# Kernel tuning notes

Hardware: AMD Instinct MI355X
Metric: run time of the kernel (lower is better)

## Reference

```python
import jax, jax.numpy as jnp
import numpy as np

H = 16   # num_heads
G = 4    # groups (code structurally requires 4)
DIM = 1024
HD = DIM // H // G  # 16


def setup_inputs() -> dict:
    key = jax.random.key(0)
    k1, k2, k3 = jax.random.split(key, 3)
    x = jax.random.normal(k1, (8, 4096, DIM), dtype=jnp.float32)
    w_qkvw = jax.random.normal(k2, (DIM, 4 * DIM), dtype=jnp.float32) * 0.02
    w_out = jax.random.normal(k3, (DIM, DIM), dtype=jnp.float32) * 0.02
    return {"x": x, "w_qkvw": w_qkvw, "w_out": w_out}


def reference(x, w_qkvw, w_out):
    B, S, dim = x.shape
    qkvw = x @ w_qkvw  # [B, S, 4*dim]
    # chunk into G groups along last dim -> G tensors of [B, S, dim] (G==4)
    chunks = jnp.split(qkvw, G, axis=-1)
    # each chunk split again into G sub-chunks of [B, S, dim/G]
    subs = [jnp.split(t, G, axis=-1) for t in chunks]
    # torch: q,k,v,w = [cat([qi,ki,vi,wi], dim=0) for qi,ki,vi,wi in zip(*subs)]
    q = jnp.concatenate([subs[i][0] for i in range(4)], axis=0)  # [4B, S, dim/G]
    k = jnp.concatenate([subs[i][1] for i in range(4)], axis=0)
    v = jnp.concatenate([subs[i][2] for i in range(4)], axis=0)
    w = jnp.concatenate([subs[i][3] for i in range(4)], axis=0)
    # faithful row-major reshape: [4B, S, dim/G] -> [4B, H, S, hd] -> transpose(1,2)
    def shp(t):
        return t.reshape(B * G, H, -1, HD).swapaxes(1, 2)  # [4B, S, H, hd]
    q, k, v = shp(q), shp(k), shp(v)
    w = w.reshape(B * G, H, -1, HD)  # [4B, H, S, hd]
    scale = HD ** -0.5
    scores = (q @ k.swapaxes(-2, -1)) * scale          # [4B, S, H, H]
    attn = jax.nn.softmax(scores, axis=-1)
    o = (attn @ v).swapaxes(1, 2).reshape(B, S, dim)   # [B, S, dim]
    return (o * w.reshape(B, S, dim)) @ w_out
```

## Files before the change

kernel.cpp:

```cpp
#include <hip/hip_runtime.h>
#include <hip/hip_bf16.h>
#include <stdint.h>


typedef __bf16 bf16;
typedef __bf16 bf16x8 __attribute__((ext_vector_type(8)));
typedef float f32x4 __attribute__((ext_vector_type(4)));

__device__ __forceinline__ void gload16(const bf16* g, bf16* l) {
  __builtin_amdgcn_global_load_lds(
      (const __attribute__((address_space(1))) void*)g,
      (__attribute__((address_space(3))) void*)l, 16, 0, 0);
}

#define BAR() asm volatile("s_barrier" ::: "memory")
#define SB() __builtin_amdgcn_sched_barrier(0)
#define LGKM0 asm volatile("s_waitcnt lgkmcnt(0)" ::: "memory")
#define PRIO1 __builtin_amdgcn_s_setprio(1)
#define PRIO0 __builtin_amdgcn_s_setprio(0)

#define READ_AX(dst, mq, AO)                                                  \
  {                                                                           \
    _Pragma("unroll") for (int i = 0; i < 4; ++i)                             \
        _Pragma("unroll") for (int kk = 0; kk < 2; ++kk)                      \
            dst[i][kk] = *(const bf16x8*)(lds + (AO) +                        \
                                          ((mq)*64 + i * 16 + fr) * 128 +     \
                                          ((kk * 64 + fkb) ^ xo));            \
  }
#define READ_B(nh, BO)                                                        \
  {                                                                           \
    _Pragma("unroll") for (int j = 0; j < 2; ++j)                             \
        _Pragma("unroll") for (int kk = 0; kk < 2; ++kk)                      \
            b[(nh)*2 + j][kk] = *(const bf16x8*)(lds + (BO) +                 \
                                                 (bro + (nh)*32 + j * 16 + fr) * 128 + \
                                                 ((kk * 64 + fkb) ^ xo));     \
  }
#define MFMA_Q(arr, mq, nh)                                                   \
  {                                                                           \
    _Pragma("unroll") for (int i = 0; i < 4; ++i)                             \
        _Pragma("unroll") for (int j = 0; j < 2; ++j) {                       \
      acc[(mq)*4 + i][(nh)*2 + j] = __builtin_amdgcn_mfma_f32_16x16x32_bf16(  \
          arr[i][0], b[(nh)*2 + j][0], acc[(mq)*4 + i][(nh)*2 + j], 0, 0, 0); \
      acc[(mq)*4 + i][(nh)*2 + j] = __builtin_amdgcn_mfma_f32_16x16x32_bf16(  \
          arr[i][1], b[(nh)*2 + j][1], acc[(mq)*4 + i][(nh)*2 + j], 0, 0, 0); \
    }                                                                         \
  }
#define STAGE_AH(h, X, base)                                                  \
  {                                                                           \
    const bf16* g = gA + ((h)*128) * 1024 + (X)*64;                           \
    gload16(g, (bf16*)(lds + (base) + (h)*16384 + wv * 1024));                \
    gload16(g + 64 * 1024, (bf16*)(lds + (base) + (h)*16384 + 8192 + wv * 1024)); \
  }
#define STAGE_BH(h, X)                                                        \
  {                                                                           \
    const int ro = 98304 + ((X)&1) * 32768 + (h)*16384;                       \
    const bf16* g = gB + ((h)*128) * 1024 + (X)*64;                           \
    gload16(g, (bf16*)(lds + ro + wv * 1024));                                \
    gload16(g + 64 * 1024, (bf16*)(lds + ro + 8192 + wv * 1024));             \
  }

template <typename OutT>
__global__ __launch_bounds__(512, 2)
void gemm256(const bf16* __restrict__ A, const bf16* __restrict__ BT,
             OutT* __restrict__ C, int N, int super) {
  constexpr int K = 1024;
  __shared__ __align__(16) char smem[163840];
  char* lds = smem;

  const int tid = threadIdx.x;
  const int lane = tid & 63;
  const int wv = tid >> 6;
  const int wr = wv >> 2;
  const int wc = wv & 3;

  const int gx = gridDim.x;
  const int nwg = gx * gridDim.y;
  const int bid = blockIdx.y * gx + blockIdx.x;
  const int xcd = bid & 7;
  const int l = bid >> 3;
  long trow, tcol;
  if (super) {
    const int s = l >> 5, i = l & 31;
    const int colS = gx >> 2;
    trow = xcd * 16 + (s / colS) * 8 + (i >> 2);
    tcol = (s % colS) * 4 + (i & 3);
  } else {
    const int swz = xcd * (nwg >> 3) + l;
    trow = swz / gx;
    tcol = swz % gx;
  }
  const long row0 = trow * 256;
  const long col0 = tcol * 256;

  const int srow = tid >> 3;
  const int scol = (((tid & 7) * 16) ^ ((srow & 7) << 4)) >> 1;
  const bf16* gA = A + (row0 + srow) * K + scol;
  const bf16* gB = BT + (col0 + srow) * K + scol;

  const int fr = lane & 15;
  const int fkb = (lane >> 4) * 16;
  const int xo = (fr & 7) << 4;
  const int bro = (wc & 1) * 64;

  bf16x8 a0[4][2], a1[4][2], b[4][2];
  f32x4 acc[8][4] = {};

  STAGE_AH(0, 0, 0); STAGE_AH(1, 0, 0);
  STAGE_BH(0, 0); STAGE_BH(1, 0);
  STAGE_AH(0, 1, 32768); STAGE_AH(1, 1, 32768);
  STAGE_BH(0, 1); STAGE_BH(1, 1);
  asm volatile("s_waitcnt vmcnt(8)" ::: "memory");
  SB(); BAR(); SB();
  READ_AX(a0, 0, wr * 16384);
  READ_B(0, 98304 + (wc >> 1) * 16384);
  SB();

  int ac0 = 0, ac1 = 32768, ac2 = 65536;
  for (int T = 0; T < 16; ++T) {
    const int aoff = ac0 + wr * 16384;
    const int aoffN = ac1 + wr * 16384;
    const int boff = 98304 + (T & 1) * 32768 + (wc >> 1) * 16384;
    const int boffN = 98304 + ((T + 1) & 1) * 32768 + (wc >> 1) * 16384;
    if (T < 14) STAGE_AH(0, T + 2, ac2);
    SB(); BAR(); LGKM0; SB();
    READ_B(1, boff); SB();
    PRIO1; MFMA_Q(a0, 0, 0); PRIO0; SB();
    if (T < 14) STAGE_AH(1, T + 2, ac2);
    SB(); BAR(); LGKM0; SB();
    PRIO1; MFMA_Q(a0, 0, 1); PRIO0; SB();
    READ_AX(a1, 1, aoff); SB();
    BAR();
    if (T < 14) {
      asm volatile("s_waitcnt vmcnt(4)" ::: "memory");
    } else if (T == 14) {
      asm volatile("s_waitcnt vmcnt(0)" ::: "memory");
    }
    LGKM0; SB();
    if (T < 14) STAGE_BH(0, T + 2);
    SB();
    PRIO1; MFMA_Q(a1, 1, 1); PRIO0; SB();
    if (T < 15) READ_AX(a0, 0, aoffN);
    SB();
    if (T < 14) STAGE_BH(1, T + 2);
    SB(); BAR(); SB();
    PRIO1; MFMA_Q(a1, 1, 0); PRIO0; SB();
    if (T < 15) READ_B(0, boffN);
    SB();
    const int t = ac0; ac0 = ac1; ac1 = ac2; ac2 = t;
  }

  const int crow = (lane >> 4) * 4;
  const int ccol = lane & 15;
  const long rb = row0 + wr * 128;
  const long cb = col0 + wc * 64;
#pragma unroll
  for (int m = 0; m < 8; ++m)
#pragma unroll
    for (int n = 0; n < 4; ++n)
#pragma unroll
      for (int i = 0; i < 4; ++i)
        C[(rb + m * 16 + crow + i) * (long)N + cb + n * 16 + ccol] =
            (OutT)acc[m][n][i];
}

__device__ __forceinline__ void load16f(const bf16* p, float* f) {
  const uint4* u = (const uint4*)p;
  uint4 a = u[0], b = u[1];
  uint32_t w[8] = {a.x, a.y, a.z, a.w, b.x, b.y, b.z, b.w};
#pragma unroll
  for (int j = 0; j < 8; ++j) {
    f[2 * j] = __uint_as_float(w[j] << 16);
    f[2 * j + 1] = __uint_as_float(w[j] & 0xffff0000u);
  }
}

__global__ __launch_bounds__(256)
void attn_fuse(const bf16* __restrict__ qkvw, bf16* __restrict__ ow,
               int b0, long bstride) {
  __shared__ bf16 data[16 * 1024];
  const int s_hi = blockIdx.x;
  const int g = blockIdx.y;
  const int bz = blockIdx.z;
  const int b = b0 + bz;
  const bf16* base = qkvw + (long)bz * bstride;
  const int tid = threadIdx.x;

#pragma unroll
  for (int i = 0; i < 8; ++i) {
    int c = tid + i * 256;
    int h = c >> 7;
    int col = (c & 127) * 8;
    *(uint4*)&data[h * 1024 + col] =
        *(const uint4*)(base + (long)(h * 256 + s_hi) * 4096 + g * 1024 + col);
  }
  __syncthreads();

  const int s_lo = tid >> 4;
  const int h1 = tid & 15;
  const int off = s_lo * 16;

  float q[16], p[16], o[16];
  load16f(&data[h1 * 1024 + off], q);

  float mx = -1e30f;
#pragma unroll
  for (int h2 = 0; h2 < 16; ++h2) {
    float kf[16];
    load16f(&data[h2 * 1024 + 256 + off], kf);
    float s = 0.f;
#pragma unroll
    for (int d = 0; d < 16; ++d) s += q[d] * kf[d];
    s *= 0.25f;
    p[h2] = s;
    mx = fmaxf(mx, s);
  }
  float sum = 0.f;
#pragma unroll
  for (int h2 = 0; h2 < 16; ++h2) {
    float e = __expf(p[h2] - mx);
    p[h2] = e;
    sum += e;
  }
  const float inv = 1.f / sum;
#pragma unroll
  for (int d = 0; d < 16; ++d) o[d] = 0.f;
#pragma unroll
  for (int h2 = 0; h2 < 16; ++h2) {
    float vf[16];
    load16f(&data[h2 * 1024 + 512 + off], vf);
    const float av = p[h2] * inv;
#pragma unroll
    for (int d = 0; d < 16; ++d) o[d] += av * vf[d];
  }
  float wf[16];
  load16f(&data[h1 * 1024 + 768 + off], wf);

  const int bp = g * 8 + b;
  const long R = (long)(bp >> 2) * 4096 + (bp & 3) * 1024 + h1 * 64 + (s_hi >> 2);
  const int cbo = (s_hi & 3) * 256 + off;
  union { uint4 u[2]; bf16 hh[16]; } st;
#pragma unroll
  for (int d = 0; d < 16; ++d) st.hh[d] = (bf16)(o[d] * wf[d]);
  uint4* dst = (uint4*)&ow[R * 1024 + cbo];
  dst[0] = st.u[0];
  dst[1] = st.u[1];
}

__global__ __launch_bounds__(256)
void cast_x_kernel(const float* __restrict__ in, bf16* __restrict__ out, long n4) {
  long i = (long)blockIdx.x * 256 + threadIdx.x;
  if (i >= n4) return;
  float4 v = ((const float4*)in)[i];
  union { uint2 d; bf16 h[4]; } r;
  r.h[0] = (bf16)v.x; r.h[1] = (bf16)v.y; r.h[2] = (bf16)v.z; r.h[3] = (bf16)v.w;
  ((uint2*)out)[i] = r.d;
}

__global__ __launch_bounds__(256)
void tcast_kernel(const float* __restrict__ in, bf16* __restrict__ out, int R, int C) {
  __shared__ float t[64][65];
  const int c0 = blockIdx.x * 64, r0 = blockIdx.y * 64;
  const int lr = threadIdx.x >> 6;
  const int lc = threadIdx.x & 63;
#pragma unroll
  for (int i = 0; i < 16; ++i)
    t[lr + i * 4][lc] = in[(long)(r0 + lr + i * 4) * C + c0 + lc];
  __syncthreads();
#pragma unroll
  for (int i = 0; i < 16; ++i) {
    int oc = lr + i * 4;
    out[(long)(c0 + oc) * R + r0 + lc] = (bf16)t[lc][oc];
  }
}

extern "C" void kernel_launch(void* const* d_in, const int* in_sizes, int n_in,
                              void* d_out, int out_size, void* d_ws, size_t ws_size,
                              hipStream_t stream) {
  const float* x = (const float*)d_in[0];
  const float* w_qkvw = (const float*)d_in[1];
  const float* w_out = (const float*)d_in[2];
  float* out = (float*)d_out;

  char* ws = (char*)d_ws;
  size_t off = 0;
  bf16* x_bf = (bf16*)(ws + off); off += (size_t)32768 * 1024 * 2;
  bf16* bt1  = (bf16*)(ws + off); off += (size_t)4096 * 1024 * 2;
  bf16* bt2  = (bf16*)(ws + off); off += (size_t)1024 * 1024 * 2;
  bf16* owb  = (bf16*)(ws + off); off += (size_t)32768 * 1024 * 2;
  bf16* qk   = (bf16*)(ws + off);
  const size_t rem = ws_size > off ? ws_size - off : 0;
  const size_t full_need = (size_t)32768 * 4096 * 2;

  cast_x_kernel<<<32768, 256, 0, stream>>>(x, x_bf, (long)8388608);
  tcast_kernel<<<dim3(64, 16), 256, 0, stream>>>(w_qkvw, bt1, 1024, 4096);
  tcast_kernel<<<dim3(16, 16), 256, 0, stream>>>(w_out, bt2, 1024, 1024);

  if (rem >= full_need) {
    gemm256<bf16><<<dim3(16, 128), 512, 0, stream>>>(x_bf, bt1, qk, 4096, 1);
    attn_fuse<<<dim3(256, 4, 8), 256, 0, stream>>>(qk, owb, 0, (long)4096 * 4096);
  } else {
    for (int b = 0; b < 8; ++b) {
      gemm256<bf16><<<dim3(16, 16), 512, 0, stream>>>(
          x_bf + (size_t)b * 4096 * 1024, bt1, qk, 4096, 0);
      attn_fuse<<<dim3(256, 4, 1), 256, 0, stream>>>(qk, owb, b, 0);
    }
  }
  gemm256<float><<<dim3(4, 128), 512, 0, stream>>>(owb, bt2, out, 1024, 1);
}
```

Measured before the change: 464.7 us.

## Restructure GEMM main loop into 8-phase ping-pong schedule with smaller LDS

Replaces the 3-stage A / 2-stage B LDS ring (160 KB) with a 2-stage double buffer for both A and B (128 KB). The K loop is unrolled by two tiles and split into eight MFMA quadrants, each followed by a barrier, with global-to-LDS staging interleaved at finer granularity. The aim is to cut LDS footprint, which may let two workgroups fit per CU, and to overlap loads with MFMA more evenly. The cost is a shallower prefetch depth and more barriers per K step, which can expose memory latency.

```diff
diff --git a/kernel.cpp b/kernel.cpp
--- a/kernel.cpp
+++ b/kernel.cpp
@@ -16,47 +16,41 @@
 #define BAR() asm volatile("s_barrier" ::: "memory")
 #define SB() __builtin_amdgcn_sched_barrier(0)
 #define LGKM0 asm volatile("s_waitcnt lgkmcnt(0)" ::: "memory")
+#define VM4 asm volatile("s_waitcnt vmcnt(4)" ::: "memory")
+#define VM0 asm volatile("s_waitcnt vmcnt(0)" ::: "memory")
 #define PRIO1 __builtin_amdgcn_s_setprio(1)
 #define PRIO0 __builtin_amdgcn_s_setprio(0)
 
-#define READ_AX(dst, mq, AO)                                                  \
+#define READ_A8(dst, base, mq)                                                \
   {                                                                           \
     _Pragma("unroll") for (int i = 0; i < 4; ++i)                             \
         _Pragma("unroll") for (int kk = 0; kk < 2; ++kk)                      \
-            dst[i][kk] = *(const bf16x8*)(lds + (AO) +                        \
+            dst[i][kk] = *(const bf16x8*)(lds + (base) + ahalf +              \
                                           ((mq)*64 + i * 16 + fr) * 128 +     \
                                           ((kk * 64 + fkb) ^ xo));            \
   }
-#define READ_B(nh, BO)                                                        \
+#define READ_B4(base, nh)                                                     \
   {                                                                           \
-    _Pragma("unroll") for (int j = 0; j < 2; ++j)                             \
+    _Pragma("unroll") for (int j2 = 0; j2 < 2; ++j2)                          \
         _Pragma("unroll") for (int kk = 0; kk < 2; ++kk)                      \
-            b[(nh)*2 + j][kk] = *(const bf16x8*)(lds + (BO) +                 \
-                                                 (bro + (nh)*32 + j * 16 + fr) * 128 + \
-                                                 ((kk * 64 + fkb) ^ xo));     \
+            b[(nh)*2 + j2][kk] = *(const bf16x8*)(lds + (base) + bhalf +      \
+                                                  (bro + (nh)*32 + j2 * 16 + fr) * 128 + \
+                                                  ((kk * 64 + fkb) ^ xo));    \
   }
 #define MFMA_Q(arr, mq, nh)                                                   \
   {                                                                           \
     _Pragma("unroll") for (int i = 0; i < 4; ++i)                             \
-        _Pragma("unroll") for (int j = 0; j < 2; ++j) {                       \
-      acc[(mq)*4 + i][(nh)*2 + j] = __builtin_amdgcn_mfma_f32_16x16x32_bf16(  \
-          arr[i][0], b[(nh)*2 + j][0], acc[(mq)*4 + i][(nh)*2 + j], 0, 0, 0); \
-      acc[(mq)*4 + i][(nh)*2 + j] = __builtin_amdgcn_mfma_f32_16x16x32_bf16(  \
-          arr[i][1], b[(nh)*2 + j][1], acc[(mq)*4 + i][(nh)*2 + j], 0, 0, 0); \
+        _Pragma("unroll") for (int j2 = 0; j2 < 2; ++j2) {                    \
+      acc[(mq)*4 + i][(nh)*2 + j2] = __builtin_amdgcn_mfma_f32_16x16x32_bf16( \
+          arr[i][0], b[(nh)*2 + j2][0], acc[(mq)*4 + i][(nh)*2 + j2], 0, 0, 0); \
+      acc[(mq)*4 + i][(nh)*2 + j2] = __builtin_amdgcn_mfma_f32_16x16x32_bf16( \
+          arr[i][1], b[(nh)*2 + j2][1], acc[(mq)*4 + i][(nh)*2 + j2], 0, 0, 0); \
     }                                                                         \
   }
-#define STAGE_AH(h, X, base)                                                  \
+#define STAGE(gsrc, lbase)                                                    \
   {                                                                           \
-    const bf16* g = gA + ((h)*128) * 1024 + (X)*64;                           \
-    gload16(g, (bf16*)(lds + (base) + (h)*16384 + wv * 1024));                \
-    gload16(g + 64 * 1024, (bf16*)(lds + (base) + (h)*16384 + 8192 + wv * 1024)); \
-  }
-#define STAGE_BH(h, X)                                                        \
-  {                                                                           \
-    const int ro = 98304 + ((X)&1) * 32768 + (h)*16384;                       \
-    const bf16* g = gB + ((h)*128) * 1024 + (X)*64;                           \
-    gload16(g, (bf16*)(lds + ro + wv * 1024));                                \
-    gload16(g + 64 * 1024, (bf16*)(lds + ro + 8192 + wv * 1024));             \
+    gload16((gsrc), (bf16*)(lds + (lbase) + wv * 1024));                      \
+    gload16((gsrc) + 64 * 1024, (bf16*)(lds + (lbase) + 8192 + wv * 1024));   \
   }
 
 template <typename OutT>
@@ -64,7 +58,7 @@
 void gemm256(const bf16* __restrict__ A, const bf16* __restrict__ BT,
              OutT* __restrict__ C, int N, int super) {
   constexpr int K = 1024;
-  __shared__ __align__(16) char smem[163840];
+  __shared__ __align__(16) char smem[131072];
   char* lds = smem;
 
   const int tid = threadIdx.x;
@@ -101,52 +95,62 @@
   const int fkb = (lane >> 4) * 16;
   const int xo = (fr & 7) << 4;
   const int bro = (wc & 1) * 64;
+  const int ahalf = wr * 16384;
+  const int bhalf = (wc >> 1) * 16384;
 
   bf16x8 a0[4][2], a1[4][2], b[4][2];
   f32x4 acc[8][4] = {};
 
-  STAGE_AH(0, 0, 0); STAGE_AH(1, 0, 0);
-  STAGE_BH(0, 0); STAGE_BH(1, 0);
-  STAGE_AH(0, 1, 32768); STAGE_AH(1, 1, 32768);
-  STAGE_BH(0, 1); STAGE_BH(1, 1);
-  asm volatile("s_waitcnt vmcnt(8)" ::: "memory");
+  STAGE(gA, 0); STAGE(gA + 131072, 16384);
+  STAGE(gB, 65536); STAGE(gB + 131072, 81920);
+  STAGE(gA + 64, 32768); STAGE(gA + 131072 + 64, 49152);
+  VM4;
   SB(); BAR(); SB();
-  READ_AX(a0, 0, wr * 16384);
-  READ_B(0, 98304 + (wc >> 1) * 16384);
-  SB();
-
-  int ac0 = 0, ac1 = 32768, ac2 = 65536;
-  for (int T = 0; T < 16; ++T) {
-    const int aoff = ac0 + wr * 16384;
-    const int aoffN = ac1 + wr * 16384;
-    const int boff = 98304 + (T & 1) * 32768 + (wc >> 1) * 16384;
-    const int boffN = 98304 + ((T + 1) & 1) * 32768 + (wc >> 1) * 16384;
-    if (T < 14) STAGE_AH(0, T + 2, ac2);
-    SB(); BAR(); LGKM0; SB();
-    READ_B(1, boff); SB();
-    PRIO1; MFMA_Q(a0, 0, 0); PRIO0; SB();
-    if (T < 14) STAGE_AH(1, T + 2, ac2);
-    SB(); BAR(); LGKM0; SB();
-    PRIO1; MFMA_Q(a0, 0, 1); PRIO0; SB();
-    READ_AX(a1, 1, aoff); SB();
-    BAR();
-    if (T < 14) {
-      asm volatile("s_waitcnt vmcnt(4)" ::: "memory");
-    } else if (T == 14) {
-      asm volatile("s_waitcnt vmcnt(0)" ::: "memory");
+
+  const bf16* gAm = gA;
+  const bf16* gBm = gB;
+  for (int j = 0; j < 8; ++j) {
+    const bool nl = (j < 7);
+    READ_A8(a0, 0, 0); READ_B4(65536, 0);
+    STAGE(gBm + 64, 98304);
+    SB(); BAR(); LGKM0; SB();
+    PRIO1; MFMA_Q(a0, 0, 0); PRIO0; SB(); BAR();
+    READ_A8(a1, 0, 1);
+    STAGE(gBm + 131072 + 64, 114688);
+    SB(); BAR(); LGKM0; SB();
+    PRIO1; MFMA_Q(a1, 1, 0); PRIO0; SB(); BAR();
+    READ_B4(65536, 1);
+    if (nl) STAGE(gAm + 128, 0);
+    SB(); BAR(); LGKM0; SB();
+    PRIO1; MFMA_Q(a1, 1, 1); PRIO0; SB(); BAR();
+    if (nl) {
+      STAGE(gAm + 131072 + 128, 16384);
+      VM4;
+    } else {
+      VM0;
     }
-    LGKM0; SB();
-    if (T < 14) STAGE_BH(0, T + 2);
-    SB();
-    PRIO1; MFMA_Q(a1, 1, 1); PRIO0; SB();
-    if (T < 15) READ_AX(a0, 0, aoffN);
-    SB();
-    if (T < 14) STAGE_BH(1, T + 2);
-    SB(); BAR(); SB();
-    PRIO1; MFMA_Q(a1, 1, 0); PRIO0; SB();
-    if (T < 15) READ_B(0, boffN);
-    SB();
-    const int t = ac0; ac0 = ac1; ac1 = ac2; ac2 = t;
+    SB(); BAR(); LGKM0; SB();
+    PRIO1; MFMA_Q(a0, 0, 1); PRIO0; SB(); BAR();
+    READ_A8(a0, 32768, 0); READ_B4(98304, 0);
+    if (nl) STAGE(gBm + 128, 65536);
+    SB(); BAR(); LGKM0; SB();
+    PRIO1; MFMA_Q(a0, 0, 0); PRIO0; SB(); BAR();
+    READ_A8(a1, 32768, 1);
+    if (nl) STAGE(gBm + 131072 + 128, 81920);
+    SB(); BAR(); LGKM0; SB();
+    PRIO1; MFMA_Q(a1, 1, 0); PRIO0; SB(); BAR();
+    READ_B4(98304, 1);
+    if (nl) STAGE(gAm + 192, 32768);
+    SB(); BAR(); LGKM0; SB();
+    PRIO1; MFMA_Q(a1, 1, 1); PRIO0; SB(); BAR();
+    if (nl) {
+      STAGE(gAm + 131072 + 192, 49152);
+      VM4;
+    }
+    SB(); BAR(); LGKM0; SB();
+    PRIO1; MFMA_Q(a0, 0, 1); PRIO0; SB(); BAR();
+    gAm += 128;
+    gBm += 128;
   }
 
   const int crow = (lane >> 4) * 4;
```

New measurement: 462.7 us. Within noise of the previous version (-0.4%).
